# Optimization experiments

Hardware: AMD Instinct MI355X
Metric: run time of the kernel (lower is better)

## Reference

```python
import jax, jax.numpy as jnp
import numpy as np

# dims: B batch, CIN/COUT channels, K kernel, H/W spatial, S stride, P padding
B, CIN, COUT, K, H, W, S, P = 8, 16, 64, 3, 32, 32, 1, 1
ALPHA, R, N_EKV, VT, VD = 0.05625, 0.1, 1.5, 0.025, 0.1


def setup_inputs() -> dict:
    key = jax.random.key(0)
    k1, k2 = jax.random.split(key)
    x = jax.random.normal(k1, (B, CIN, H, W), dtype=jnp.float32)
    # torch init: uniform_(theta, 1.0, 8.0)
    theta = jax.random.uniform(k2, (COUT, CIN * K * K), dtype=jnp.float32, minval=1.0, maxval=8.0)
    scale = jnp.array(1.0, dtype=jnp.float32)
    return {"x": x, "theta": theta, "scale": scale}


def _unfold(x, k, s, p):
    # torch.nn.Unfold: patches flattened channel-major as (C, kh, kw)
    b, c, h, w = x.shape
    ho = (h + 2 * p - k) // s + 1
    wo = (w + 2 * p - k) // s + 1
    xp = jnp.pad(x, ((0, 0), (0, 0), (p, p), (p, p)))
    patches = jnp.stack(
        [xp[:, :, i:i + ho * s:s, j:j + wo * s:s] for i in range(k) for j in range(k)],
        axis=2,
    )  # (B, C, K*K, Ho, Wo)
    return patches.reshape(b, c * k * k, ho * wo), ho, wo


def _log1p_exp_stable_sq(a):
    # clamp to [-50, 20] then softplus; squared (EKV f)
    a = jnp.clip(a, -50.0, 20.0)
    sp = jnp.log1p(jnp.exp(a))
    return sp * sp


def reference(x, theta, scale):
    theta = jnp.clip(theta, 1.0, 8.0)  # mirrors theta.data.clamp_(1, 8)
    vg, ho, wo = _unfold(x, K, S, P)          # (B, Cin*K^2, L)
    vg = vg[:, None, :, :]                    # (B, 1, Cin*K^2, L)
    vth = theta[None, :, :, None]             # (1, Cout, Cin*K^2, 1)
    denom = 2.0 * N_EKV * VT
    term1 = _log1p_exp_stable_sq((vg - vth) / denom)
    term2 = _log1p_exp_stable_sq((vg - vth - VD) / denom)
    currents = jnp.clip(ALPHA * (term1 - term2), 0.0, None)
    i_k = jnp.sum(currents, axis=2)           # reduce over Cin*K^2 -> (B, Cout, L)
    v_out = i_k * R * scale
    return v_out.reshape(x.shape[0], COUT, ho, wo)
```

## Files before the change

kernel.cpp:

```cpp
#include <hip/hip_runtime.h>

#define BB 8
#define CIN 16
#define COUT 64
#define HH 32
#define WW 32
#define PH 34
#define PW 34
#define PPLANE (PH * PW)

#define SCALE_C 19.235933878519388f
#define K2E 0.26359713811472845f
#define B_HI 28.85390081777927f
#define OUT_CONST (0.4804530139182014f * 0.05625f * 0.1f)

#define EXP2F(x) __builtin_amdgcn_exp2f(x)
#define LOG2F(x) __builtin_amdgcn_logf(x)

#define NTH (COUT * CIN * 9)

__global__ __launch_bounds__(256) void init_kernel(const float* __restrict__ x,
                                                   const float* __restrict__ theta,
                                                   float* __restrict__ xp,
                                                   float* __restrict__ thp) {
    if (blockIdx.x < 578) {
        int idx = blockIdx.x * 256 + threadIdx.x;
        int c = idx / PPLANE;
        int r = idx - c * PPLANE;
        int y = r / PW;
        int xc = r - y * PW;
        float v = 0.0f;
        if (y >= 1 && y <= HH && xc >= 1 && xc <= WW) {
            v = x[c * (HH * WW) + (y - 1) * WW + (xc - 1)] * SCALE_C;
        }
        xp[idx] = v;
    } else {
        int i = (blockIdx.x - 578) * 256 + threadIdx.x;
        if (i < NTH) {
            thp[i] = fminf(fmaxf(theta[i], 1.0f), 8.0f) * SCALE_C;
        }
    }
}

__device__ __forceinline__ void load9(const float* __restrict__ p, float* v) {
#pragma unroll
    for (int dy = 0; dy < 3; ++dy)
#pragma unroll
        for (int dx = 0; dx < 3; ++dx)
            v[dy * 3 + dx] = p[dy * PW + dx];
}

__device__ __forceinline__ void compute9(const float* v, const float* __restrict__ thp,
                                         float* acc) {
#pragma unroll
    for (int k = 0; k < 9; ++k) {
        float b1 = v[k] - thp[k];
        float e1 = EXP2F(b1);
        float e2 = e1 * K2E;
        float l1 = fminf(LOG2F(1.0f + e1), B_HI);
        float l2 = fminf(LOG2F(1.0f + e2), B_HI);
        float a = acc[k % 3];
        a = fmaf(l1, l1, a);
        a = fmaf(-l2, l2, a);
        acc[k % 3] = a;
    }
}

__global__ __launch_bounds__(256, 8) void ekv_kernel(const float* __restrict__ xp,
                                                     const float* __restrict__ thp,
                                                     const float* __restrict__ scale,
                                                     float* __restrict__ out) {
    int bid = blockIdx.x;
    int b = bid & 7;
    int tile = (bid >> 3) & 3;
    int co = (bid >> 8) * 8 + ((bid >> 5) & 7);

    int t = threadIdx.x;
    int ow = t & 31;
    int oh = tile * 8 + (t >> 5);

    const float* thc = thp + co * (CIN * 9);
    const float* p0 = xp + (size_t)b * (CIN * PPLANE) + oh * PW + ow;

    float acc[3] = {0.0f, 0.0f, 0.0f};

    float va[9], vb[9];
    load9(p0, va);
#pragma unroll 1
    for (int cin = 0; cin < CIN; cin += 2) {
        load9(p0 + (cin + 1) * PPLANE, vb);
        compute9(va, thc + cin * 9, acc);
        int nc = cin + 2 < CIN ? cin + 2 : CIN - 1;
        load9(p0 + nc * PPLANE, va);
        compute9(vb, thc + (cin + 1) * 9, acc);
    }

    float sc = scale[0] * (OUT_CONST);
    out[(((size_t)b * COUT + co) * HH + oh) * WW + ow] =
        (acc[0] + acc[1] + acc[2]) * sc;
}

extern "C" void kernel_launch(void* const* d_in, const int* in_sizes, int n_in,
                              void* d_out, int out_size, void* d_ws, size_t ws_size,
                              hipStream_t stream) {
    const float* x = (const float*)d_in[0];
    const float* theta = (const float*)d_in[1];
    const float* scale = (const float*)d_in[2];
    float* out = (float*)d_out;

    float* thp = (float*)d_ws;
    float* xp = thp + NTH;
    (void)ws_size;

    init_kernel<<<578 + (NTH + 255) / 256, 256, 0, stream>>>(x, theta, xp, thp);
    ekv_kernel<<<BB * 4 * COUT, 256, 0, stream>>>(xp, thp, scale, out);
}
```

Before: 86.64 us.

## Skip negligible EKV terms per wave and use vector row loads with padded planes

Widens the padded input row pitch to 36 floats so each 3-tap row is fetched with one 16-byte load instead of three scalar loads. It also adds a wave-wide vote that skips the exp/log evaluation for a tap when every lane's scaled difference is below a threshold. Below that threshold the softplus-squared difference contributes a negligible amount. This trades divergence checks and a slight approximation for fewer transcendental ops. The padded stores in init remain aligned only if the row pitch stays a multiple of four floats, but the per-thread base offset (ow) makes the 16-byte loads unaligned for most lanes.

```diff
diff --git a/kernel.cpp b/kernel.cpp
--- a/kernel.cpp
+++ b/kernel.cpp
@@ -6,24 +6,26 @@
 #define HH 32
 #define WW 32
 #define PH 34
-#define PW 34
+#define PW 36
 #define PPLANE (PH * PW)
 
 #define SCALE_C 19.235933878519388f
 #define K2E 0.26359713811472845f
 #define B_HI 28.85390081777927f
+#define WINLO_S (-13.849872392533959f)
 #define OUT_CONST (0.4804530139182014f * 0.05625f * 0.1f)
 
 #define EXP2F(x) __builtin_amdgcn_exp2f(x)
 #define LOG2F(x) __builtin_amdgcn_logf(x)
 
 #define NTH (COUT * CIN * 9)
+#define PAD_ELEMS (BB * CIN * PPLANE)
 
 __global__ __launch_bounds__(256) void init_kernel(const float* __restrict__ x,
                                                    const float* __restrict__ theta,
                                                    float* __restrict__ xp,
                                                    float* __restrict__ thp) {
-    if (blockIdx.x < 578) {
+    if (blockIdx.x < 612) {
         int idx = blockIdx.x * 256 + threadIdx.x;
         int c = idx / PPLANE;
         int r = idx - c * PPLANE;
@@ -35,34 +37,38 @@
         }
         xp[idx] = v;
     } else {
-        int i = (blockIdx.x - 578) * 256 + threadIdx.x;
+        int i = (blockIdx.x - 612) * 256 + threadIdx.x;
         if (i < NTH) {
             thp[i] = fminf(fmaxf(theta[i], 1.0f), 8.0f) * SCALE_C;
         }
     }
 }
 
-__device__ __forceinline__ void load9(const float* __restrict__ p, float* v) {
+__device__ __forceinline__ void load12(const float* __restrict__ p, float4* v) {
 #pragma unroll
     for (int dy = 0; dy < 3; ++dy)
-#pragma unroll
-        for (int dx = 0; dx < 3; ++dx)
-            v[dy * 3 + dx] = p[dy * PW + dx];
+        __builtin_memcpy(&v[dy], p + dy * PW, 16);
 }
 
-__device__ __forceinline__ void compute9(const float* v, const float* __restrict__ thp,
+__device__ __forceinline__ void compute9(const float4* v, const float* __restrict__ thp,
                                          float* acc) {
 #pragma unroll
-    for (int k = 0; k < 9; ++k) {
-        float b1 = v[k] - thp[k];
-        float e1 = EXP2F(b1);
-        float e2 = e1 * K2E;
-        float l1 = fminf(LOG2F(1.0f + e1), B_HI);
-        float l2 = fminf(LOG2F(1.0f + e2), B_HI);
-        float a = acc[k % 3];
-        a = fmaf(l1, l1, a);
-        a = fmaf(-l2, l2, a);
-        acc[k % 3] = a;
+    for (int dy = 0; dy < 3; ++dy) {
+        float row[3] = {v[dy].x, v[dy].y, v[dy].z};
+#pragma unroll
+        for (int dx = 0; dx < 3; ++dx) {
+            float b1 = row[dx] - thp[dy * 3 + dx];
+            if (__any(b1 > WINLO_S)) {
+                float e1 = EXP2F(b1);
+                float e2 = e1 * K2E;
+                float l1 = fminf(LOG2F(1.0f + e1), B_HI);
+                float l2 = fminf(LOG2F(1.0f + e2), B_HI);
+                float a = acc[dx];
+                a = fmaf(l1, l1, a);
+                a = fmaf(-l2, l2, a);
+                acc[dx] = a;
+            }
+        }
     }
 }
 
@@ -84,14 +90,14 @@
 
     float acc[3] = {0.0f, 0.0f, 0.0f};
 
-    float va[9], vb[9];
-    load9(p0, va);
+    float4 va[3], vb[3];
+    load12(p0, va);
 #pragma unroll 1
     for (int cin = 0; cin < CIN; cin += 2) {
-        load9(p0 + (cin + 1) * PPLANE, vb);
+        load12(p0 + (cin + 1) * PPLANE, vb);
         compute9(va, thc + cin * 9, acc);
         int nc = cin + 2 < CIN ? cin + 2 : CIN - 1;
-        load9(p0 + nc * PPLANE, va);
+        load12(p0 + nc * PPLANE, va);
         compute9(vb, thc + (cin + 1) * 9, acc);
     }
 
@@ -112,6 +118,6 @@
     float* xp = thp + NTH;
     (void)ws_size;
 
-    init_kernel<<<578 + (NTH + 255) / 256, 256, 0, stream>>>(x, theta, xp, thp);
+    init_kernel<<<612 + (NTH + 255) / 256, 256, 0, stream>>>(x, theta, xp, thp);
     ekv_kernel<<<BB * 4 * COUT, 256, 0, stream>>>(xp, thp, scale, out);
 }
```

Measured after the change: 74.77 us. 1.16x faster.
